# Kernel tuning notes

Hardware: AMD Instinct MI355X
Metric: run time of the kernel (lower is better)

The kernel has to match this reference:

```python
import jax, jax.numpy as jnp
import numpy as np

MULT = 32       # multiplicity per irrep type (both input and output)
N = 262144      # number of nodes/examples
LS = (0, 1, 2, 3)  # irrep degrees -> block sizes 2l+1 = 1,3,5,7


def setup_inputs() -> dict:
    key = jax.random.key(0)
    keys = jax.random.split(key, 2 * len(LS))
    inp = {}
    for j, l in enumerate(LS):
        m = 2 * l + 1
        inp[f"x{l}"] = jax.random.normal(keys[2 * j], (N, MULT, m), dtype=jnp.float32)
        inp[f"W{l}"] = jax.random.normal(keys[2 * j + 1], (MULT, MULT, m), dtype=jnp.float32)
    return inp


def reference(x0, x1, x2, x3, W0, W1, W2, W3):
    # Block-diagonal equivariant linear: for each irrep type l,
    # out[n, o, m] = sum_i W_l[o, i, m] * x_l[n, i, m]
    # (elementwise in m within each 2l+1 block, summed over input multiplicity i).
    outs = [
        jnp.einsum("nim,oim->nom", x, W)
        for x, W in ((x0, W0), (x1, W1), (x2, W2), (x3, W3))
    ]
    # Concatenate flattened irrep blocks -> [N, MULT*(1+3+5+7)] = [N, 512]
    return jnp.concatenate([o.reshape(o.shape[0], -1) for o in outs], axis=-1)
```

## Files before the change

kernel.cpp:

```cpp
#include <hip/hip_runtime.h>
#include <hip/hip_fp16.h>


#define NTH 512
#define TN  32

typedef _Float16 f16x8 __attribute__((ext_vector_type(8)));
typedef float    f32x4 __attribute__((ext_vector_type(4)));

#define LGKM0_BAR() do { asm volatile("s_waitcnt lgkmcnt(0)" ::: "memory"); \
                         __builtin_amdgcn_s_barrier(); } while (0)

template<int M_, int PB>
__device__ __forceinline__ void stageW(const float* __restrict__ src,
                                       __half* __restrict__ dst, int tid)
{
    #pragma unroll
    for (int it = 0; it < (256 * M_ + NTH - 1) / NTH; ++it) {
        const int f = tid + it * NTH;
        if (f < 256 * M_) {
            float4 v = ((const float4*)src)[f];
            const float vf[4] = {v.x, v.y, v.z, v.w};
            const int e0 = 4 * f;
            #pragma unroll
            for (int k = 0; k < 4; ++k) {
                const int e = e0 + k;
                const int o = e / (32 * M_);
                const int r = e - o * (32 * M_);
                const int i = r / M_, mi = r - i * M_;
                dst[(PB + mi) * 1280 + o * 40 + i] = __float2half(vf[k]);
            }
        }
    }
}

template<int M_, int PB>
__device__ __forceinline__ void mkoff(int tloc, int* offk)
{
    const int e0    = 4 * tloc;
    const int nodel = e0 / (32 * M_);
    const int r0    = e0 - nodel * (32 * M_);
    #pragma unroll
    for (int k = 0; k < 4; ++k) {
        const int ii = (r0 + k) / M_, mi = (r0 + k) - ii * M_;
        offk[k] = (PB + mi) * 1280 + nodel * 40 + ii;
    }
}

__device__ __forceinline__ void plane_info(int p, int& Mm, int& BASE, int& MI)
{
    if (p == 0)     { Mm = 1; BASE = 0;   MI = 0;     }
    else if (p < 4) { Mm = 3; BASE = 32;  MI = p - 1; }
    else if (p < 9) { Mm = 5; BASE = 128; MI = p - 4; }
    else            { Mm = 7; BASE = 288; MI = p - 9; }
}

__global__ __launch_bounds__(NTH, 4) void eqlin(
    const float* __restrict__ x0, const float* __restrict__ x1,
    const float* __restrict__ x2, const float* __restrict__ x3,
    const float* __restrict__ w0, const float* __restrict__ w1,
    const float* __restrict__ w2, const float* __restrict__ w3,
    float* __restrict__ out, int n_tiles)
{
    __shared__ __align__(16) __half XT[20480];
    __shared__ __align__(16) __half WT[20480];
    const int tid  = threadIdx.x;
    const int wave = tid >> 6;
    const int lane = tid & 63;

    int thrg, Mg, offk[4];
    const float* xb;
    bool isM1 = false;
    if (tid < 32)       { thrg = 32;  Mg = 1; xb = x0; mkoff<1, 0>(tid,       offk); isM1 = true; }
    else if (tid < 128) { thrg = 96;  Mg = 3; xb = x1; mkoff<3, 1>(tid - 32,  offk); }
    else if (tid < 288) { thrg = 160; Mg = 5; xb = x2; mkoff<5, 4>(tid - 128, offk); }
    else                { thrg = 224; Mg = 7; xb = x3; mkoff<7, 9>(tid - 288, offk); }
    const int  tloc    = (tid < 32) ? tid : (tid < 128) ? tid - 32 : (tid < 288) ? tid - 128 : tid - 288;
    const long jstride = 4L * thrg;
    const long tstride = (long)gridDim.x * 1024L * Mg;

    const float* srcp = xb + (long)blockIdx.x * (1024L * Mg) + 4 * tloc;
    float4 pf[8];
    #pragma unroll
    for (int j = 0; j < 8; ++j)
        pf[j] = *(const float4*)(srcp + j * jstride);

    stageW<1, 0>(w0, WT, tid);
    stageW<3, 1>(w1, WT, tid);
    stageW<5, 4>(w2, WT, tid);
    stageW<7, 9>(w3, WT, tid);

    int Mm0, BASE0, MI0, Mm1, BASE1, MI1;
    plane_info(wave * 2,     Mm0, BASE0, MI0);
    plane_info(wave * 2 + 1, Mm1, BASE1, MI1);
    const int lrow = lane & 15;
    const int lk8  = (lane >> 4) * 8;
    const int crow = (lane >> 4) * 4;

    for (int t = blockIdx.x; t < n_tiles; t += gridDim.x) {
        const long node0 = (long)t * TN;

        LGKM0_BAR();

        #pragma unroll
        for (int j = 0; j < 8; ++j) {
            const float4 v = pf[j];
            const int jb = j * 160;
            if (isM1) {
                __half2* p = (__half2*)&XT[offk[0] + jb];
                p[0] = __floats2half2_rn(v.x, v.y);
                p[1] = __floats2half2_rn(v.z, v.w);
            } else {
                XT[offk[0] + jb] = __float2half(v.x);
                XT[offk[1] + jb] = __float2half(v.y);
                XT[offk[2] + jb] = __float2half(v.z);
                XT[offk[3] + jb] = __float2half(v.w);
            }
        }

        if (t + (long)gridDim.x < n_tiles) {
            srcp += tstride;
            #pragma unroll
            for (int j = 0; j < 8; ++j)
                pf[j] = *(const float4*)(srcp + j * jstride);
        }

        LGKM0_BAR();

        f32x4 acc[2][2][2] = {};
        #pragma unroll
        for (int pl = 0; pl < 2; ++pl) {
            const int plane = wave * 2 + pl;
            const __half* xp = XT + plane * 1280 + lrow * 40 + lk8;
            const __half* wp = WT + plane * 1280 + lrow * 40 + lk8;
            f16x8 A0 = *(const f16x8*)xp;
            f16x8 A1 = *(const f16x8*)(xp + 640);
            f16x8 B0 = *(const f16x8*)wp;
            f16x8 B1 = *(const f16x8*)(wp + 640);
            acc[pl][0][0] = __builtin_amdgcn_mfma_f32_16x16x32_f16(A0, B0, acc[pl][0][0], 0, 0, 0);
            acc[pl][0][1] = __builtin_amdgcn_mfma_f32_16x16x32_f16(A0, B1, acc[pl][0][1], 0, 0, 0);
            acc[pl][1][0] = __builtin_amdgcn_mfma_f32_16x16x32_f16(A1, B0, acc[pl][1][0], 0, 0, 0);
            acc[pl][1][1] = __builtin_amdgcn_mfma_f32_16x16x32_f16(A1, B1, acc[pl][1][1], 0, 0, 0);
        }

        LGKM0_BAR();

        __half* OUT = XT;
        #pragma unroll
        for (int pl = 0; pl < 2; ++pl) {
            const int Mm   = pl ? Mm1   : Mm0;
            const int BASE = pl ? BASE1 : BASE0;
            const int MI   = pl ? MI1   : MI0;
            #pragma unroll
            for (int nh = 0; nh < 2; ++nh)
            #pragma unroll
            for (int oh = 0; oh < 2; ++oh) {
                const int o     = oh * 16 + lrow;
                const int colb  = BASE + o * Mm + MI;
                const int nodeb = nh * 16 + crow;
                #pragma unroll
                for (int r = 0; r < 4; ++r)
                    OUT[(nodeb + r) * 520 + colb] = __float2half(acc[pl][nh][oh][r]);
            }
        }

        LGKM0_BAR();

        float* dst = out + node0 * 512;
        #pragma unroll
        for (int it = 0; it < 4; ++it) {
            const int d0   = 8 * tid + 4096 * it;
            const int node = d0 >> 9, col = d0 & 511;
            uint4 h8 = *(const uint4*)(OUT + node * 520 + col);
            const __half2* hp = (const __half2*)&h8;
            float2 f0 = __half22float2(hp[0]);
            float2 f1 = __half22float2(hp[1]);
            float2 f2 = __half22float2(hp[2]);
            float2 f3 = __half22float2(hp[3]);
            *(float4*)(dst + d0)     = make_float4(f0.x, f0.y, f1.x, f1.y);
            *(float4*)(dst + d0 + 4) = make_float4(f2.x, f2.y, f3.x, f3.y);
        }
    }
}

extern "C" void kernel_launch(void* const* d_in, const int* in_sizes, int n_in,
                              void* d_out, int out_size, void* d_ws, size_t ws_size,
                              hipStream_t stream)
{
    long tot = 0;
    for (int i = 0; i < n_in; ++i) tot += in_sizes[i];
    const long N = (tot - 16384) / 512;
    const int  ms[4] = {1, 3, 5, 7};
    const float* xs[4]  = {nullptr, nullptr, nullptr, nullptr};
    const float* wsp[4] = {nullptr, nullptr, nullptr, nullptr};
    for (int i = 0; i < n_in; ++i) {
        const long s = in_sizes[i];
        for (int l = 0; l < 4; ++l) {
            if (s == N * 32 * ms[l])      xs[l]  = (const float*)d_in[i];
            else if (s == 1024L * ms[l])  wsp[l] = (const float*)d_in[i];
        }
    }
    const int n_tiles = (int)(N / TN);
    const int grid = 512;
    hipLaunchKernelGGL(eqlin, dim3(grid), dim3(NTH), 0, stream,
                       xs[0], xs[1], xs[2], xs[3],
                       wsp[0], wsp[1], wsp[2], wsp[3],
                       (float*)d_out, n_tiles);
}
```

Measured before the change: 217.0 us.

## Keep weight fragments in registers and defer output store to overlap next tile

Weight MFMA fragments are loaded from LDS once into registers before the tile loop, so the separate W buffer is dropped and replaced by a dedicated output staging buffer. The global store of the previous tile's output is moved after the next tile's LDS staging and prefetch, and the loop now uses two barriers per tile instead of four. The goal is less LDS traffic and fewer barriers, with output writes overlapping compute. In exchange, register pressure rises by 16 VGPRs per lane and LDS use shrinks. Correctness relies on the write-then-read ordering across the remaining barriers.

```diff
diff --git a/kernel.cpp b/kernel.cpp
--- a/kernel.cpp
+++ b/kernel.cpp
@@ -63,7 +63,7 @@
     float* __restrict__ out, int n_tiles)
 {
     __shared__ __align__(16) __half XT[20480];
-    __shared__ __align__(16) __half WT[20480];
+    __shared__ __align__(16) __half OC[16640];
     const int tid  = threadIdx.x;
     const int wave = tid >> 6;
     const int lane = tid & 63;
@@ -85,22 +85,33 @@
     for (int j = 0; j < 8; ++j)
         pf[j] = *(const float4*)(srcp + j * jstride);
 
-    stageW<1, 0>(w0, WT, tid);
-    stageW<3, 1>(w1, WT, tid);
-    stageW<5, 4>(w2, WT, tid);
-    stageW<7, 9>(w3, WT, tid);
+    stageW<1, 0>(w0, XT, tid);
+    stageW<3, 1>(w1, XT, tid);
+    stageW<5, 4>(w2, XT, tid);
+    stageW<7, 9>(w3, XT, tid);
+
+    const int lrow = lane & 15;
+    const int lk8  = (lane >> 4) * 8;
+    const int crow = (lane >> 4) * 4;
+
+    LGKM0_BAR();
+    f16x8 Wf[2][2];
+    {
+        const __half* wb = XT + (wave * 2) * 1280 + lrow * 40 + lk8;
+        Wf[0][0] = *(const f16x8*)wb;
+        Wf[0][1] = *(const f16x8*)(wb + 640);
+        Wf[1][0] = *(const f16x8*)(wb + 1280);
+        Wf[1][1] = *(const f16x8*)(wb + 1920);
+    }
+    LGKM0_BAR();
 
     int Mm0, BASE0, MI0, Mm1, BASE1, MI1;
     plane_info(wave * 2,     Mm0, BASE0, MI0);
     plane_info(wave * 2 + 1, Mm1, BASE1, MI1);
-    const int lrow = lane & 15;
-    const int lk8  = (lane >> 4) * 8;
-    const int crow = (lane >> 4) * 4;
-
+
+    long prev_node0 = -1;
     for (int t = blockIdx.x; t < n_tiles; t += gridDim.x) {
         const long node0 = (long)t * TN;
-
-        LGKM0_BAR();
 
         #pragma unroll
         for (int j = 0; j < 8; ++j) {
@@ -117,12 +128,27 @@
                 XT[offk[3] + jb] = __float2half(v.w);
             }
         }
-
         if (t + (long)gridDim.x < n_tiles) {
             srcp += tstride;
             #pragma unroll
             for (int j = 0; j < 8; ++j)
                 pf[j] = *(const float4*)(srcp + j * jstride);
+        }
+        if (prev_node0 >= 0) {
+            float* dst = out + prev_node0 * 512;
+            #pragma unroll
+            for (int it = 0; it < 4; ++it) {
+                const int d0   = 8 * tid + 4096 * it;
+                const int node = d0 >> 9, col = d0 & 511;
+                uint4 h8 = *(const uint4*)(OC + node * 520 + col);
+                const __half2* hp = (const __half2*)&h8;
+                float2 f0 = __half22float2(hp[0]);
+                float2 f1 = __half22float2(hp[1]);
+                float2 f2 = __half22float2(hp[2]);
+                float2 f3 = __half22float2(hp[3]);
+                *(float4*)(dst + d0)     = make_float4(f0.x, f0.y, f1.x, f1.y);
+                *(float4*)(dst + d0 + 4) = make_float4(f2.x, f2.y, f3.x, f3.y);
+            }
         }
 
         LGKM0_BAR();
@@ -132,20 +158,13 @@
         for (int pl = 0; pl < 2; ++pl) {
             const int plane = wave * 2 + pl;
             const __half* xp = XT + plane * 1280 + lrow * 40 + lk8;
-            const __half* wp = WT + plane * 1280 + lrow * 40 + lk8;
             f16x8 A0 = *(const f16x8*)xp;
             f16x8 A1 = *(const f16x8*)(xp + 640);
-            f16x8 B0 = *(const f16x8*)wp;
-            f16x8 B1 = *(const f16x8*)(wp + 640);
-            acc[pl][0][0] = __builtin_amdgcn_mfma_f32_16x16x32_f16(A0, B0, acc[pl][0][0], 0, 0, 0);
-            acc[pl][0][1] = __builtin_amdgcn_mfma_f32_16x16x32_f16(A0, B1, acc[pl][0][1], 0, 0, 0);
-            acc[pl][1][0] = __builtin_amdgcn_mfma_f32_16x16x32_f16(A1, B0, acc[pl][1][0], 0, 0, 0);
-            acc[pl][1][1] = __builtin_amdgcn_mfma_f32_16x16x32_f16(A1, B1, acc[pl][1][1], 0, 0, 0);
-        }
-
-        LGKM0_BAR();
-
-        __half* OUT = XT;
+            acc[pl][0][0] = __builtin_amdgcn_mfma_f32_16x16x32_f16(A0, Wf[pl][0], acc[pl][0][0], 0, 0, 0);
+            acc[pl][0][1] = __builtin_amdgcn_mfma_f32_16x16x32_f16(A0, Wf[pl][1], acc[pl][0][1], 0, 0, 0);
+            acc[pl][1][0] = __builtin_amdgcn_mfma_f32_16x16x32_f16(A1, Wf[pl][0], acc[pl][1][0], 0, 0, 0);
+            acc[pl][1][1] = __builtin_amdgcn_mfma_f32_16x16x32_f16(A1, Wf[pl][1], acc[pl][1][1], 0, 0, 0);
+        }
         #pragma unroll
         for (int pl = 0; pl < 2; ++pl) {
             const int Mm   = pl ? Mm1   : Mm0;
@@ -160,18 +179,21 @@
                 const int nodeb = nh * 16 + crow;
                 #pragma unroll
                 for (int r = 0; r < 4; ++r)
-                    OUT[(nodeb + r) * 520 + colb] = __float2half(acc[pl][nh][oh][r]);
+                    OC[(nodeb + r) * 520 + colb] = __float2half(acc[pl][nh][oh][r]);
             }
         }
 
         LGKM0_BAR();
-
-        float* dst = out + node0 * 512;
+        prev_node0 = node0;
+    }
+
+    if (prev_node0 >= 0) {
+        float* dst = out + prev_node0 * 512;
         #pragma unroll
         for (int it = 0; it < 4; ++it) {
             const int d0   = 8 * tid + 4096 * it;
             const int node = d0 >> 9, col = d0 & 511;
-            uint4 h8 = *(const uint4*)(OUT + node * 520 + col);
+            uint4 h8 = *(const uint4*)(OC + node * 520 + col);
             const __half2* hp = (const __half2*)&h8;
             float2 f0 = __half22float2(hp[0]);
             float2 f1 = __half22float2(hp[1]);
```

Result: faster. 210.2 us (-3.2%).
